# Performance work log

Hardware: AMD Instinct MI355X
Metric: run time of the kernel (lower is better)

Reference implementation:

```python
import jax, jax.numpy as jnp
import numpy as np

N, M, NTYPES, C, AXIS = 4096, 128, 2, 64, 16
TYPE_IDX = (0, 2048, 4096)        # atom-type partition along center axis
NTYPE_IDX = (0, 64, 128)          # neighbor-type partition along neighbor axis
RCUT = 6.0
BOX = 20.0
SR_MEAN = (0.1, 0.1)              # precomputed stats (get_stats)
SR_STD = (0.05, 0.05)
NORM = 20.0                       # avg neighbor count + 1


def setup_inputs() -> dict:
    key = jax.random.key(0)
    ks = jax.random.split(key, 16)
    coord_3N = jax.random.uniform(ks[0], (3, N), dtype=jnp.float32) * BOX
    box = jnp.full((3,), BOX, dtype=jnp.float32)
    # neighbors sorted by type: first 64 of type 0, last 64 of type 1
    nbr0 = jax.random.randint(ks[1], (N, M // 2), 0, TYPE_IDX[1])
    nbr1 = jax.random.randint(ks[2], (N, M // 2), TYPE_IDX[1], TYPE_IDX[2])
    nbrs_idx = jnp.concatenate([nbr0, nbr1], axis=1).astype(jnp.int32)
    # 4 per-(center,neighbor)-type embedding nets, widths 1->16->32->64, stacked
    eW0 = jax.random.normal(ks[3], (4, 1, 16), dtype=jnp.float32)
    eb0 = jax.random.normal(ks[4], (4, 16), dtype=jnp.float32) * 0.1
    eW1 = jax.random.normal(ks[5], (4, 16, 32), dtype=jnp.float32) / 4.0
    eb1 = jax.random.normal(ks[6], (4, 32), dtype=jnp.float32) * 0.1
    eW2 = jax.random.normal(ks[7], (4, 32, 64), dtype=jnp.float32) / (32.0 ** 0.5)
    eb2 = jax.random.normal(ks[8], (4, 64), dtype=jnp.float32) * 0.1
    Tbias = jnp.zeros((1, C), dtype=jnp.float32)
    # 2 per-type fitting nets, widths 1024->128->128->1, stacked
    fW0 = jax.random.normal(ks[9], (2, AXIS * C, 128), dtype=jnp.float32) / (AXIS * C) ** 0.5
    fb0 = jnp.zeros((2, 128), dtype=jnp.float32)
    fW1 = jax.random.normal(ks[10], (2, 128, 128), dtype=jnp.float32) / (128.0 ** 0.5)
    fb1 = jnp.zeros((2, 128), dtype=jnp.float32)
    fW2 = jax.random.normal(ks[11], (2, 128, 1), dtype=jnp.float32) / (128.0 ** 0.5)
    fb2 = jnp.zeros((2, 1), dtype=jnp.float32)
    Ebias = jnp.zeros((2,), dtype=jnp.float32)
    return {"coord_3N": coord_3N, "box": box, "nbrs_idx": nbrs_idx,
            "eW0": eW0, "eb0": eb0, "eW1": eW1, "eb1": eb1, "eW2": eW2, "eb2": eb2,
            "Tbias": Tbias, "fW0": fW0, "fb0": fb0, "fW1": fW1, "fb1": fb1,
            "fW2": fW2, "fb2": fb2, "Ebias": Ebias}


def reference(coord_3N, box, nbrs_idx, eW0, eb0, eW1, eb1, eW2, eb2,
              Tbias, fW0, fb0, fW1, fb1, fW2, fb2, Ebias):
    # --- neighbor gather + minimal-image relative coords (get_relative_coord) ---
    x_3NM = coord_3N[:, nbrs_idx] - coord_3N[:, :, None]            # [3,N,M]
    x_3NM = x_3NM - box[:, None, None] * jnp.round(x_3NM / box[:, None, None])
    r2 = (x_3NM ** 2).sum(0)
    mask = r2 > 1e-12
    rsafe = jnp.sqrt(jnp.where(mask, r2, 1.0))                      # safe for grads
    r_NM = jnp.where(mask, rsafe, 0.0)                              # [N,M]
    # --- smooth radial feature sr(r) = switch(r)/r ---
    sw = 0.5 * jnp.cos(jnp.pi * jnp.minimum(r_NM, RCUT) / RCUT) + 0.5
    sr_NM = jnp.where(mask & (r_NM < RCUT), sw / rsafe, 0.0)
    # --- per-center-type normalization (slice_t / concat_t over type_idx) ---
    srn_rows, srcn = [], []
    for i in range(NTYPES):
        blk = sr_NM[TYPE_IDX[i]:TYPE_IDX[i + 1]]
        srn_rows.append(blk / SR_STD[i])
        srcn.append((blk - SR_MEAN[i]) / SR_STD[i])
    sr_norm_NM = jnp.concatenate(srn_rows, 0)
    x_norm_3NM = x_3NM / jnp.where(mask, rsafe, 1.0)[None]
    R_3NM = 3 ** 0.5 * sr_norm_NM * x_norm_3NM
    R2diag_3NM = 9 ** 0.5 * sr_norm_NM * (x_norm_3NM ** 2 - 1.0 / 3.0)
    R2offd_3NM = 18 ** 0.5 * sr_norm_NM * (x_norm_3NM * jnp.stack([x_norm_3NM[1], x_norm_3NM[2], x_norm_3NM[0]]))
    R_XNM = jnp.concatenate([sr_norm_NM[None], R_3NM, R2diag_3NM, R2offd_3NM])  # [10,N,M]

    # --- per-(center,neighbor)-type embedding MLPs on scalar sr feature ---
    def embed(x, k):  # x: [n, m] -> [n, m, C]
        h = jnp.tanh(x[:, :, None] @ eW0[k] + eb0[k])
        h = jnp.tanh(h @ eW1[k] + eb1[k])
        return jnp.tanh(h @ eW2[k] + eb2[k])

    rows = []
    for i in range(NTYPES):
        cols = [embed(srcn[i][:, NTYPE_IDX[j]:NTYPE_IDX[j + 1]], i * NTYPES + j)
                for j in range(NTYPES)]
        rows.append(jnp.concatenate(cols, 1))
    embed_NMC = jnp.concatenate(rows, 0)                            # [N,M,C]

    # --- descriptor contraction ---
    T_NXC = jnp.einsum('xnm,nmc->nxc', R_XNM, embed_NMC) / NORM     # [N,10,C]
    T_NC = T_NXC[:, 0] + Tbias
    T_N3C = T_NXC[:, 1:4]
    T_N6C = T_NXC[:, 4:]
    G_NAC = T_NC[:, None] * T_NC[:, :AXIS, None] \
        + (T_N3C[:, :, None] * T_N3C[:, :, :AXIS, None]).sum(1)     # [N,AXIS,C]
    # use_2nd branch
    G1 = T_N3C[:, :, AXIS:2 * AXIS]                                 # [N,3,AXIS]
    G11 = jnp.concatenate([G1 ** 2,
                           2 ** 0.5 * G1 * jnp.stack([G1[:, 1], G1[:, 2], G1[:, 0]], axis=1)], axis=1)
    G2 = G11 + T_N6C[:, :, AXIS:2 * AXIS]                           # [N,6,AXIS]
    G_NAC = G_NAC + jnp.einsum('nxa,nxc->nac', G2, T_N6C)

    # --- per-type fitting nets ---
    Gflat = G_NAC.reshape(N, AXIS * C)
    energy = jnp.zeros((), dtype=Gflat.dtype)
    for t in range(NTYPES):
        g = Gflat[TYPE_IDX[t]:TYPE_IDX[t + 1]]
        h = jnp.tanh(g @ fW0[t] + fb0[t])
        h = jnp.tanh(h @ fW1[t] + fb1[t])
        f = h @ fW2[t] + fb2[t]
        energy = energy + (f + Ebias[t]).sum()
    return energy
```

## Files before the change

kernel.cpp:

```cpp
#include <hip/hip_runtime.h>
#include <hip/hip_fp16.h>

typedef _Float16 h16;
typedef h16 v2h __attribute__((ext_vector_type(2)));
typedef h16 v8h __attribute__((ext_vector_type(8)));
typedef float f4 __attribute__((ext_vector_type(4)));

#define NATOM 4096
#define HALF_N 2048
#define K2 2.885390081777927f
#define GSCL 0.015625f
#define W0SCL (64.0f * K2)

#define TBL_N 2048
#define W0MIN_ (-0.201f)
#define DW_ (1.2005f / 2047.0f)
#define RSCALE_ (2047.0f / 1.2005f)

__device__ __forceinline__ float rcp_fast(float x) {
#if __has_builtin(__builtin_amdgcn_rcpf)
  return __builtin_amdgcn_rcpf(x);
#else
  return 1.0f / x;
#endif
}

__device__ __forceinline__ float exp2_fast(float x) {
#if __has_builtin(__builtin_amdgcn_exp2f)
  return __builtin_amdgcn_exp2f(x);
#else
  return exp2f(x);
#endif
}

__device__ __forceinline__ float tanh_e2(float d) {
  float r = rcp_fast(1.0f + exp2_fast(d));
  return fmaf(-2.0f, r, 1.0f);
}

__device__ __forceinline__ v8h lds_v8h(const h16* base, int byte) {
  return *(const v8h*)((const char*)base + byte);
}

__global__ __launch_bounds__(256) void k_setup(
    const float* __restrict__ eW0, const float* __restrict__ eb0,
    const float* __restrict__ eW1, const float* __restrict__ eb1,
    const float* __restrict__ eW2, const float* __restrict__ eb2,
    const float* __restrict__ fW0, const float* __restrict__ fW1,
    const float* __restrict__ coord,
    h16* __restrict__ tbl, h16* __restrict__ W0t, h16* __restrict__ W1t,
    f4* __restrict__ coordP)
{
  const int bid = blockIdx.x, tid = threadIdx.x;
  if (bid < 512) {
    __shared__ float sW1[512];
    __shared__ float sW2[2048];
    __shared__ float sW0s[16], sb0s[16], sb1s[32], sb2s[64];
    const int net = bid >> 7;
    for (int i = tid; i < 512; i += 256) sW1[i] = eW1[net * 512 + i];
    for (int i = tid; i < 2048; i += 256) sW2[i] = eW2[net * 2048 + i];
    if (tid < 16) { sW0s[tid] = eW0[net * 16 + tid]; sb0s[tid] = eb0[net * 16 + tid]; }
    else if (tid >= 32 && tid < 64) sb1s[tid - 32] = eb1[net * 32 + tid - 32];
    else if (tid >= 64 && tid < 128) sb2s[tid - 64] = eb2[net * 64 + tid - 64];
    __syncthreads();

    const int u = (bid & 127) * 256 + tid;
    const int e = u >> 4, cq = u & 15;
    const float w = W0MIN_ + (float)e * DW_;
    const float s = 8.0f * w * rcp_fast(1.0f - fabsf(w));
    float h0[16];
#pragma unroll
    for (int i = 0; i < 16; ++i)
      h0[i] = tanh_e2(K2 * fmaf(s, sW0s[i], sb0s[i]));
    float h1[32];
#pragma unroll
    for (int j = 0; j < 32; ++j) {
      float a = sb1s[j];
#pragma unroll
      for (int i = 0; i < 16; ++i) a = fmaf(h0[i], sW1[i * 32 + j], a);
      h1[j] = tanh_e2(K2 * a);
    }
    f4 a4 = *(const f4*)&sb2s[cq * 4];
    for (int j = 0; j < 32; ++j) {
      f4 wv4 = *(const f4*)&sW2[j * 64 + cq * 4];
      a4 += h1[j] * wv4;
    }
    union { h16 e4[4]; unsigned long long q; } o;
#pragma unroll
    for (int q = 0; q < 4; ++q) o.e4[q] = (h16)tanh_e2(K2 * a4[q]);
    *(unsigned long long*)&tbl[((size_t)(net * TBL_N + e)) * 64 + cq * 4] = o.q;
  } else if (bid < 640) {
    int idx = (bid - 512) * 256 + tid;
    int t = idx >> 14, n = idx & 127, k8 = (idx >> 7) & 127;
    union { v8h v; h16 e[8]; } o;
#pragma unroll
    for (int i = 0; i < 8; ++i)
      o.e[i] = (h16)(W0SCL * fW0[(size_t)t * 131072 + (size_t)(k8 * 8 + i) * 128 + n]);
    *(v8h*)&W0t[((size_t)t * 128 + n) * 1024 + k8 * 8] = o.v;
  } else if (bid < 656) {
    int idx = (bid - 640) * 256 + tid;
    f4 c;
    c.x = coord[idx]; c.y = coord[NATOM + idx]; c.z = coord[2 * NATOM + idx];
    c.w = 0.0f;
    coordP[idx] = c;
  } else {
    int idx = (bid - 656) * 256 + tid;
    int t = idx >> 11, rem = idx & 2047;
    int n = rem >> 4, k8 = rem & 15;
    union { v8h v; h16 e[8]; } o;
#pragma unroll
    for (int i = 0; i < 8; ++i)
      o.e[i] = (h16)(K2 * fW1[(size_t)t * 16384 + (size_t)(k8 * 8 + i) * 128 + n]);
    *(v8h*)&W1t[((size_t)t * 128 + n) * 128 + k8 * 8] = o.v;
  }
}

__global__ __launch_bounds__(256, 2) void k_embed(
    const f4* __restrict__ coordP, const float* __restrict__ box,
    const int* __restrict__ nbrs, const float* __restrict__ Tbias,
    const h16* __restrict__ tbl, h16* __restrict__ Gout)
{
  __shared__ h16   E32t[4][64][40] __attribute__((aligned(16)));
  __shared__ h16   Rls[4][10][136] __attribute__((aligned(16)));
  __shared__ float Tls[4][10][64];

  const int tid = threadIdx.x;
  const int wv = tid >> 6;
  const int lane = tid & 63;
  const int n = blockIdx.x * 4 + wv;
  const int ti = (n >= HALF_N) ? 1 : 0;
  const int c15 = lane & 15, g4 = lane >> 4;
  const int mloc = lane >> 1, hh = lane & 1;

  const int jnb0 = nbrs[(size_t)n * 128 + lane];
  const int jnb1 = nbrs[(size_t)n * 128 + 64 + lane];

  int uf0 = 0, uf1 = 0;
  {
    const float bx = box[0], by = box[1], bz = box[2];
    const float rbx = rcp_fast(bx), rby = rcp_fast(by), rbz = rcp_fast(bz);
    const f4 cme = coordP[n];
#pragma unroll
    for (int nb = 0; nb < 2; ++nb) {
      const int m = nb * 64 + lane;
      const f4 cj = coordP[nb ? jnb1 : jnb0];
      float dx = cj.x - cme.x;
      float dy = cj.y - cme.y;
      float dz = cj.z - cme.z;
      dx -= bx * rintf(dx * rbx);
      dy -= by * rintf(dy * rby);
      dz -= bz * rintf(dz * rbz);
      float r2 = dx * dx + dy * dy + dz * dz;
      bool mk = r2 > 1e-12f;
      float rs = sqrtf(mk ? r2 : 1.0f);
      float r  = mk ? rs : 0.0f;
      float sw = 0.5f * __cosf(0.52359878f * fminf(r, 6.0f)) + 0.5f;
      float invr = mk ? rcp_fast(rs) : 1.0f;
      float sr = (mk && r < 6.0f) ? sw * invr : 0.0f;
      float x0 = dx * invr, x1 = dy * invr, x2 = dz * invr;
      float srn = sr * 20.0f;
      float s   = (sr - 0.1f) * 20.0f;
      Rls[wv][0][m] = (h16)srn;
      Rls[wv][1][m] = (h16)(1.7320508f * srn * x0);
      Rls[wv][2][m] = (h16)(1.7320508f * srn * x1);
      Rls[wv][3][m] = (h16)(1.7320508f * srn * x2);
      Rls[wv][4][m] = (h16)(3.0f * srn * (x0 * x0 - 0.33333334f));
      Rls[wv][5][m] = (h16)(3.0f * srn * (x1 * x1 - 0.33333334f));
      Rls[wv][6][m] = (h16)(3.0f * srn * (x2 * x2 - 0.33333334f));
      Rls[wv][7][m] = (h16)(4.2426407f * srn * (x0 * x1));
      Rls[wv][8][m] = (h16)(4.2426407f * srn * (x1 * x2));
      Rls[wv][9][m] = (h16)(4.2426407f * srn * (x2 * x0));
      float wr = s * rcp_fast(8.0f + fabsf(s));
      float fidx = (wr - W0MIN_) * RSCALE_;
      fidx = fminf(fmaxf(fidx, 0.0f), 2045.99f);
      float i0f = floorf(fidx);
      h16 frh = (h16)(fidx - i0f);
      int uf = ((int)i0f << 16) |
               (int)__builtin_bit_cast(unsigned short, frh);
      if (nb == 0) uf0 = uf; else uf1 = uf;
    }
  }

  union U8 { v8h v; v2h p[4]; h16 e[8]; };
  const int rrow = (c15 < 10) ? c15 : 9;
  const v8h vzero = {};
  f4 tac[4];
#pragma unroll
  for (int nt = 0; nt < 4; ++nt) tac[nt] = (f4){0.f, 0.f, 0.f, 0.f};

  auto issue = [&](int ks, U8* buf) -> float {
    unsigned uu = (unsigned)__builtin_amdgcn_ds_bpermute(
        (((ks & 1) * 32) + mloc) * 4, (ks < 2) ? uf0 : uf1);
    int i0 = (int)(uu >> 16);
    float fr = (float)__builtin_bit_cast(h16, (unsigned short)(uu & 0xffffu));
    const int net = ti * 2 + (ks >> 1);
    const h16* rp = tbl + ((size_t)net * TBL_N + i0) * 64 + hh * 8;
#pragma unroll
    for (int q = 0; q < 4; ++q) {
      buf[q].v     = *(const v8h*)(rp + q * 16);
      buf[4 + q].v = *(const v8h*)(rp + 64 + q * 16);
    }
    return fr;
  };

  auto proc = [&](int ks, U8* buf, float fr) {
    v2h fr2; fr2.x = (h16)fr; fr2.y = (h16)fr;
#pragma unroll
    for (int q = 0; q < 4; ++q) {
#pragma unroll
      for (int p = 0; p < 4; ++p) {
        v2h d = buf[4 + q].p[p] - buf[q].p[p];
        v2h e2 = buf[q].p[p] + fr2 * d;
        const int ch = q * 16 + hh * 8 + p * 2;
        E32t[wv][ch][mloc]     = e2.x;
        E32t[wv][ch + 1][mloc] = e2.y;
      }
    }
    v8h ra = *(const v8h*)&Rls[wv][rrow][ks * 32 + g4 * 8];
    if (c15 >= 10) ra = vzero;
#pragma unroll
    for (int nt = 0; nt < 4; ++nt) {
      v8h bf = *(const v8h*)&E32t[wv][nt * 16 + c15][g4 * 8];
      tac[nt] = __builtin_amdgcn_mfma_f32_16x16x32_f16(ra, bf, tac[nt], 0, 0, 0);
    }
  };

  U8 bA[8], bB[8];
  float frA = issue(0, bA);
  float frB = issue(1, bB);
  proc(0, bA, frA);
  frA = issue(2, bA);
  proc(1, bB, frB);
  frB = issue(3, bB);
  proc(2, bA, frA);
  proc(3, bB, frB);

#pragma unroll
  for (int nt = 0; nt < 4; ++nt)
#pragma unroll
    for (int r = 0; r < 4; ++r) {
      int x = g4 * 4 + r;
      if (x < 10) Tls[wv][x][nt * 16 + c15] = tac[nt][r] * 0.05f;
    }

  {
    const int c = lane;
    const float tnc  = Tls[wv][0][c] + Tbias[c];
    const float t3c0 = Tls[wv][1][c], t3c1 = Tls[wv][2][c], t3c2 = Tls[wv][3][c];
    const float t6c0 = Tls[wv][4][c], t6c1 = Tls[wv][5][c], t6c2 = Tls[wv][6][c];
    const float t6c3 = Tls[wv][7][c], t6c4 = Tls[wv][8][c], t6c5 = Tls[wv][9][c];
    h16* gp = Gout + (size_t)n * 1024;
#pragma unroll
    for (int a = 0; a < 16; ++a) {
      float g = tnc * (Tls[wv][0][a] + Tbias[a]);
      g += t3c0 * Tls[wv][1][a] + t3c1 * Tls[wv][2][a] + t3c2 * Tls[wv][3][a];
      const float g1x = Tls[wv][1][16 + a], g1y = Tls[wv][2][16 + a], g1z = Tls[wv][3][16 + a];
      g += (g1x * g1x + Tls[wv][4][16 + a]) * t6c0;
      g += (g1y * g1y + Tls[wv][5][16 + a]) * t6c1;
      g += (g1z * g1z + Tls[wv][6][16 + a]) * t6c2;
      g += (1.4142135f * g1x * g1y + Tls[wv][7][16 + a]) * t6c3;
      g += (1.4142135f * g1y * g1z + Tls[wv][8][16 + a]) * t6c4;
      g += (1.4142135f * g1z * g1x + Tls[wv][9][16 + a]) * t6c5;
      gp[a * 64 + c] = (h16)(g * GSCL);
    }
  }
}

__global__ __launch_bounds__(256) void k_fit(
    const h16* __restrict__ G16, const h16* __restrict__ W0t,
    const h16* __restrict__ W1t,
    const float* __restrict__ fb0, const float* __restrict__ fb1,
    const float* __restrict__ fW2, const float* __restrict__ fb2,
    const float* __restrict__ Ebias, float* __restrict__ BP)
{
  __shared__ h16 As[2][32][64]  __attribute__((aligned(16)));
  __shared__ h16 Bs[2][128][64] __attribute__((aligned(16)));
  __shared__ h16 ht[32][128]    __attribute__((aligned(16)));
  __shared__ h16 W1s[128][128]  __attribute__((aligned(16)));
  __shared__ float red[32][33];

  const int tid = threadIdx.x;
  const int abase = blockIdx.x * 32;
  const int t = (abase >= HALF_N) ? 1 : 0;
  const int lane = tid & 63, w = tid >> 6;
  const int c15 = lane & 15, g4 = lane >> 4;
  const int rt = w & 1, ng = w >> 1;

  float fb0v[4], b1v[4], w2v[4];
#pragma unroll
  for (int nt = 0; nt < 4; ++nt) {
    const int nn = ng * 64 + nt * 16 + c15;
    fb0v[nt] = K2 * fb0[t * 128 + nn];
    b1v[nt]  = K2 * fb1[t * 128 + nn];
    w2v[nt]  = fW2[t * 128 + nn];
  }

#pragma unroll
  for (int u = 0; u < 8; ++u) {
    int idx = u * 256 + tid;
    int nrow = idx >> 4, c8 = idx & 15;
    v8h v = *(const v8h*)&W1t[((size_t)t * 128 + nrow) * 128 + c8 * 8];
    int byte = nrow * 256 + ((c8 * 16) ^ ((nrow & 7) << 4));
    *(v8h*)((char*)&W1s[0][0] + byte) = v;
  }

  f4 acc[4];
#pragma unroll
  for (int nt = 0; nt < 4; ++nt) acc[nt] = (f4){0.f, 0.f, 0.f, 0.f};

  auto stageK = [&](int kc, int p) {
    {
      int r = tid >> 3, c8 = tid & 7;
      v8h v = *(const v8h*)&G16[(size_t)(abase + r) * 1024 + kc * 64 + c8 * 8];
      int byte = r * 128 + ((c8 * 16) ^ ((r & 7) << 4));
      *(v8h*)((char*)&As[p][0][0] + byte) = v;
    }
#pragma unroll
    for (int u = 0; u < 4; ++u) {
      int idx = u * 256 + tid;
      int nrow = idx >> 3, c8 = idx & 7;
      v8h v = *(const v8h*)&W0t[((size_t)t * 128 + nrow) * 1024 + kc * 64 + c8 * 8];
      int byte = nrow * 128 + ((c8 * 16) ^ ((nrow & 7) << 4));
      *(v8h*)((char*)&Bs[p][0][0] + byte) = v;
    }
  };

  stageK(0, 0);
  __syncthreads();
  for (int kc = 0; kc < 16; ++kc) {
    const int p = kc & 1;
    if (kc < 15) stageK(kc + 1, p ^ 1);
#pragma unroll
    for (int ksub = 0; ksub < 2; ++ksub) {
      const int ar = rt * 16 + c15;
      const int koff = (ksub * 32 + g4 * 8) * 2;
      v8h a = lds_v8h(&As[p][0][0], ar * 128 + (koff ^ ((ar & 7) << 4)));
#pragma unroll
      for (int nt = 0; nt < 4; ++nt) {
        const int br = ng * 64 + nt * 16 + c15;
        v8h b = lds_v8h(&Bs[p][0][0], br * 128 + (koff ^ ((br & 7) << 4)));
        acc[nt] = __builtin_amdgcn_mfma_f32_16x16x32_f16(a, b, acc[nt], 0, 0, 0);
      }
    }
    __syncthreads();
  }

#pragma unroll
  for (int nt = 0; nt < 4; ++nt)
#pragma unroll
    for (int r = 0; r < 4; ++r) {
      int a = rt * 16 + g4 * 4 + r;
      int k = ng * 64 + nt * 16 + c15;
      h16 hv = (h16)tanh_e2(acc[nt][r] + fb0v[nt]);
      int byte = a * 256 + ((k * 2) ^ ((a & 7) << 4));
      *((h16*)((char*)&ht[0][0] + byte)) = hv;
    }
  __syncthreads();

  f4 acc2[4];
#pragma unroll
  for (int nt = 0; nt < 4; ++nt) acc2[nt] = (f4){0.f, 0.f, 0.f, 0.f};
#pragma unroll
  for (int ks2 = 0; ks2 < 4; ++ks2) {
    const int ar = rt * 16 + c15;
    const int koff = (ks2 * 32 + g4 * 8) * 2;
    v8h a = lds_v8h(&ht[0][0], ar * 256 + (koff ^ ((ar & 7) << 4)));
#pragma unroll
    for (int nt = 0; nt < 4; ++nt) {
      const int br = ng * 64 + nt * 16 + c15;
      v8h b = lds_v8h(&W1s[0][0], br * 256 + (koff ^ ((br & 7) << 4)));
      acc2[nt] = __builtin_amdgcn_mfma_f32_16x16x32_f16(a, b, acc2[nt], 0, 0, 0);
    }
  }

#pragma unroll
  for (int r = 0; r < 4; ++r) {
    float v = 0.0f;
#pragma unroll
    for (int nt = 0; nt < 4; ++nt)
      v += tanh_e2(acc2[nt][r] + b1v[nt]) * w2v[nt];
    red[rt * 16 + g4 * 4 + r][ng * 16 + c15] = v;
  }
  __syncthreads();
  if (tid < 64) {
    const int a = tid & 31, half = tid >> 5;
    float s = 0.0f;
#pragma unroll
    for (int c = 0; c < 16; ++c) s += red[a][half * 16 + c];
    s += __shfl_xor(s, 32);
    s += __shfl_xor(s, 16);
    s += __shfl_xor(s, 8);
    s += __shfl_xor(s, 4);
    s += __shfl_xor(s, 2);
    s += __shfl_xor(s, 1);
    if (tid == 0) BP[blockIdx.x] = s + 32.0f * (fb2[t] + Ebias[t]);
  }
}

__global__ __launch_bounds__(64) void k_reduce(const float* __restrict__ BP,
                                               float* __restrict__ out)
{
  int tid = threadIdx.x;
  float s = BP[tid] + BP[tid + 64];
  s += __shfl_xor(s, 32);
  s += __shfl_xor(s, 16);
  s += __shfl_xor(s, 8);
  s += __shfl_xor(s, 4);
  s += __shfl_xor(s, 2);
  s += __shfl_xor(s, 1);
  if (tid == 0) out[0] = s;
}

extern "C" void kernel_launch(void* const* d_in, const int* in_sizes, int n_in,
                              void* d_out, int out_size, void* d_ws, size_t ws_size,
                              hipStream_t stream) {
  const float* coord = (const float*)d_in[0];
  const float* box   = (const float*)d_in[1];
  const int*   nbrs  = (const int*)d_in[2];
  const float* eW0   = (const float*)d_in[3];
  const float* eb0   = (const float*)d_in[4];
  const float* eW1   = (const float*)d_in[5];
  const float* eb1   = (const float*)d_in[6];
  const float* eW2   = (const float*)d_in[7];
  const float* eb2   = (const float*)d_in[8];
  const float* Tbias = (const float*)d_in[9];
  const float* fW0   = (const float*)d_in[10];
  const float* fb0   = (const float*)d_in[11];
  const float* fW1   = (const float*)d_in[12];
  const float* fb1   = (const float*)d_in[13];
  const float* fW2   = (const float*)d_in[14];
  const float* fb2   = (const float*)d_in[15];
  const float* Ebias = (const float*)d_in[16];

  char* ws = (char*)d_ws;
  h16*   G16 = (h16*)ws;
  h16*   W0t = (h16*)(ws + (size_t)8  * 1024 * 1024);
  h16*   W1t = (h16*)(ws + (size_t)9  * 1024 * 1024);
  h16*   tbl = (h16*)(ws + (size_t)10 * 1024 * 1024);
  f4*    cP  = (f4*)(ws + (size_t)11 * 1024 * 1024);
  float* BP  = (float*)(ws + (size_t)12 * 1024 * 1024);

  k_setup<<<672, 256, 0, stream>>>(eW0, eb0, eW1, eb1, eW2, eb2, fW0, fW1,
                                   coord, tbl, W0t, W1t, cP);
  k_embed<<<1024, 256, 0, stream>>>(cP, box, nbrs, Tbias, tbl, G16);
  k_fit<<<128, 256, 0, stream>>>(G16, W0t, W1t, fb0, fb1, fW2, fb2, Ebias, BP);
  k_reduce<<<1, 64, 0, stream>>>(BP, (float*)d_out);
}
```

Before: 44.84 us.

## Compute G descriptor contraction with MFMA and shrink embed kernel LDS footprint

The per-atom G = T^T·U contraction (16x64 from 10 inner terms) moves from a scalar FP32 loop over LDS into a single-wave fp16 MFMA. T and a scaled U matrix are packed into reused LDS pools. LDS is consolidated into two per-wave pools, occupancy is raised to 4 blocks per CU, and the table interpolation is remapped so each lane handles two neighbors and 16 channels, allowing paired v2h stores. The tradeoff is extra fp16 rounding of T and U, which needs the USCL scaling to stay in range.

```diff
diff --git a/kernel.cpp b/kernel.cpp
--- a/kernel.cpp
+++ b/kernel.cpp
@@ -3,6 +3,7 @@
 
 typedef _Float16 h16;
 typedef h16 v2h __attribute__((ext_vector_type(2)));
+typedef h16 v4h __attribute__((ext_vector_type(4)));
 typedef h16 v8h __attribute__((ext_vector_type(8)));
 typedef float f4 __attribute__((ext_vector_type(4)));
 
@@ -11,6 +12,8 @@
 #define K2 2.885390081777927f
 #define GSCL 0.015625f
 #define W0SCL (64.0f * K2)
+#define USCL 0.0625f
+#define GOUTS (GSCL / USCL)
 
 #define TBL_N 2048
 #define W0MIN_ (-0.201f)
@@ -115,14 +118,13 @@
   }
 }
 
-__global__ __launch_bounds__(256, 2) void k_embed(
+__global__ __launch_bounds__(256, 4) void k_embed(
     const f4* __restrict__ coordP, const float* __restrict__ box,
     const int* __restrict__ nbrs, const float* __restrict__ Tbias,
     const h16* __restrict__ tbl, h16* __restrict__ Gout)
 {
-  __shared__ h16   E32t[4][64][40] __attribute__((aligned(16)));
-  __shared__ h16   Rls[4][10][136] __attribute__((aligned(16)));
-  __shared__ float Tls[4][10][64];
+  __shared__ h16 pool1[4][2560] __attribute__((aligned(16)));
+  __shared__ h16 pool2[4][1360] __attribute__((aligned(16)));
 
   const int tid = threadIdx.x;
   const int wv = tid >> 6;
@@ -130,7 +132,10 @@
   const int n = blockIdx.x * 4 + wv;
   const int ti = (n >= HALF_N) ? 1 : 0;
   const int c15 = lane & 15, g4 = lane >> 4;
-  const int mloc = lane >> 1, hh = lane & 1;
+  const int mp = lane >> 2, cg = lane & 3;
+
+  h16* E32 = &pool1[wv][0];
+  h16* Rl  = &pool2[wv][0];
 
   const int jnb0 = nbrs[(size_t)n * 128 + lane];
   const int jnb1 = nbrs[(size_t)n * 128 + 64 + lane];
@@ -160,16 +165,16 @@
       float x0 = dx * invr, x1 = dy * invr, x2 = dz * invr;
       float srn = sr * 20.0f;
       float s   = (sr - 0.1f) * 20.0f;
-      Rls[wv][0][m] = (h16)srn;
-      Rls[wv][1][m] = (h16)(1.7320508f * srn * x0);
-      Rls[wv][2][m] = (h16)(1.7320508f * srn * x1);
-      Rls[wv][3][m] = (h16)(1.7320508f * srn * x2);
-      Rls[wv][4][m] = (h16)(3.0f * srn * (x0 * x0 - 0.33333334f));
-      Rls[wv][5][m] = (h16)(3.0f * srn * (x1 * x1 - 0.33333334f));
-      Rls[wv][6][m] = (h16)(3.0f * srn * (x2 * x2 - 0.33333334f));
-      Rls[wv][7][m] = (h16)(4.2426407f * srn * (x0 * x1));
-      Rls[wv][8][m] = (h16)(4.2426407f * srn * (x1 * x2));
-      Rls[wv][9][m] = (h16)(4.2426407f * srn * (x2 * x0));
+      Rl[0 * 136 + m] = (h16)srn;
+      Rl[1 * 136 + m] = (h16)(1.7320508f * srn * x0);
+      Rl[2 * 136 + m] = (h16)(1.7320508f * srn * x1);
+      Rl[3 * 136 + m] = (h16)(1.7320508f * srn * x2);
+      Rl[4 * 136 + m] = (h16)(3.0f * srn * (x0 * x0 - 0.33333334f));
+      Rl[5 * 136 + m] = (h16)(3.0f * srn * (x1 * x1 - 0.33333334f));
+      Rl[6 * 136 + m] = (h16)(3.0f * srn * (x2 * x2 - 0.33333334f));
+      Rl[7 * 136 + m] = (h16)(4.2426407f * srn * (x0 * x1));
+      Rl[8 * 136 + m] = (h16)(4.2426407f * srn * (x1 * x2));
+      Rl[9 * 136 + m] = (h16)(4.2426407f * srn * (x2 * x0));
       float wr = s * rcp_fast(8.0f + fabsf(s));
       float fidx = (wr - W0MIN_) * RSCALE_;
       fidx = fminf(fmaxf(fidx, 0.0f), 2045.99f);
@@ -188,80 +193,117 @@
 #pragma unroll
   for (int nt = 0; nt < 4; ++nt) tac[nt] = (f4){0.f, 0.f, 0.f, 0.f};
 
-  auto issue = [&](int ks, U8* buf) -> float {
-    unsigned uu = (unsigned)__builtin_amdgcn_ds_bpermute(
-        (((ks & 1) * 32) + mloc) * 4, (ks < 2) ? uf0 : uf1);
-    int i0 = (int)(uu >> 16);
-    float fr = (float)__builtin_bit_cast(h16, (unsigned short)(uu & 0xffffu));
-    const int net = ti * 2 + (ks >> 1);
-    const h16* rp = tbl + ((size_t)net * TBL_N + i0) * 64 + hh * 8;
-#pragma unroll
-    for (int q = 0; q < 4; ++q) {
-      buf[q].v     = *(const v8h*)(rp + q * 16);
-      buf[4 + q].v = *(const v8h*)(rp + 64 + q * 16);
-    }
-    return fr;
+  auto issue = [&](int ks, U8* buf, float* fr) {
+#pragma unroll
+    for (int e = 0; e < 2; ++e) {
+      int src = ((ks & 1) * 32 + mp * 2 + e) * 4;
+      unsigned uu = (unsigned)__builtin_amdgcn_ds_bpermute(src, (ks < 2) ? uf0 : uf1);
+      int i0 = (int)(uu >> 16);
+      fr[e] = (float)__builtin_bit_cast(h16, (unsigned short)(uu & 0xffffu));
+      const int net = ti * 2 + (ks >> 1);
+      const h16* rp = tbl + ((size_t)net * TBL_N + i0) * 64 + cg * 16;
+      buf[e * 4 + 0].v = *(const v8h*)(rp);
+      buf[e * 4 + 1].v = *(const v8h*)(rp + 8);
+      buf[e * 4 + 2].v = *(const v8h*)(rp + 64);
+      buf[e * 4 + 3].v = *(const v8h*)(rp + 72);
+    }
   };
 
-  auto proc = [&](int ks, U8* buf, float fr) {
-    v2h fr2; fr2.x = (h16)fr; fr2.y = (h16)fr;
-#pragma unroll
-    for (int q = 0; q < 4; ++q) {
+  auto proc = [&](int ks, U8* buf, const float* fr) {
+    v2h f0; f0.x = (h16)fr[0]; f0.y = (h16)fr[0];
+    v2h f1; f1.x = (h16)fr[1]; f1.y = (h16)fr[1];
+    const int m0 = mp * 2;
+#pragma unroll
+    for (int ch8 = 0; ch8 < 2; ++ch8) {
 #pragma unroll
       for (int p = 0; p < 4; ++p) {
-        v2h d = buf[4 + q].p[p] - buf[q].p[p];
-        v2h e2 = buf[q].p[p] + fr2 * d;
-        const int ch = q * 16 + hh * 8 + p * 2;
-        E32t[wv][ch][mloc]     = e2.x;
-        E32t[wv][ch + 1][mloc] = e2.y;
+        v2h e0 = buf[ch8].p[p]     + f0 * (buf[2 + ch8].p[p] - buf[ch8].p[p]);
+        v2h e1 = buf[4 + ch8].p[p] + f1 * (buf[6 + ch8].p[p] - buf[4 + ch8].p[p]);
+        const int c = cg * 16 + ch8 * 8 + p * 2;
+        v2h w0; w0.x = e0.x; w0.y = e1.x;
+        v2h w1; w1.x = e0.y; w1.y = e1.y;
+        *(v2h*)&E32[c * 40 + m0]       = w0;
+        *(v2h*)&E32[(c + 1) * 40 + m0] = w1;
       }
     }
-    v8h ra = *(const v8h*)&Rls[wv][rrow][ks * 32 + g4 * 8];
+    v8h ra = *(const v8h*)&Rl[rrow * 136 + ks * 32 + g4 * 8];
     if (c15 >= 10) ra = vzero;
 #pragma unroll
     for (int nt = 0; nt < 4; ++nt) {
-      v8h bf = *(const v8h*)&E32t[wv][nt * 16 + c15][g4 * 8];
+      v8h bf = *(const v8h*)&E32[(nt * 16 + c15) * 40 + g4 * 8];
       tac[nt] = __builtin_amdgcn_mfma_f32_16x16x32_f16(ra, bf, tac[nt], 0, 0, 0);
     }
   };
 
   U8 bA[8], bB[8];
-  float frA = issue(0, bA);
-  float frB = issue(1, bB);
+  float frA[2], frB[2];
+  issue(0, bA, frA);
+  issue(1, bB, frB);
   proc(0, bA, frA);
-  frA = issue(2, bA);
+  issue(2, bA, frA);
   proc(1, bB, frB);
-  frB = issue(3, bB);
+  issue(3, bB, frB);
   proc(2, bA, frA);
   proc(3, bB, frB);
 
-#pragma unroll
-  for (int nt = 0; nt < 4; ++nt)
-#pragma unroll
-    for (int r = 0; r < 4; ++r) {
-      int x = g4 * 4 + r;
-      if (x < 10) Tls[wv][x][nt * 16 + c15] = tac[nt][r] * 0.05f;
-    }
+  h16* Vt = E32;
+  h16* Ul = Rl;
+#pragma unroll
+  for (int nt = 0; nt < 4; ++nt) {
+    const int col = nt * 16 + c15;
+    float tb = (g4 == 0) ? Tbias[col] : 0.0f;
+    v4h pk;
+    pk[0] = (h16)(tac[nt][0] * 0.05f + tb);
+    pk[1] = (h16)(tac[nt][1] * 0.05f);
+    pk[2] = (h16)(tac[nt][2] * 0.05f);
+    pk[3] = (h16)(tac[nt][3] * 0.05f);
+    *(v4h*)&Vt[col * 40 + g4 * 4] = pk;
+  }
+  *(v8h*)&Vt[lane * 40 + 16] = vzero;
+  *(v8h*)&Vt[lane * 40 + 24] = vzero;
+
+  if (lane < 16) {
+    const h16* va = &Vt[lane * 40];
+    const h16* vb = &Vt[(16 + lane) * 40];
+    v8h Ta = *(const v8h*)va;
+    v8h Tb = *(const v8h*)vb;
+    v2h Tb8 = *(const v2h*)(vb + 8);
+    float g1x = (float)Tb[1], g1y = (float)Tb[2], g1z = (float)Tb[3];
+    v8h up;
+    up[0] = (h16)((float)Ta[0] * USCL);
+    up[1] = (h16)((float)Ta[1] * USCL);
+    up[2] = (h16)((float)Ta[2] * USCL);
+    up[3] = (h16)((float)Ta[3] * USCL);
+    up[4] = (h16)((g1x * g1x + (float)Tb[4]) * USCL);
+    up[5] = (h16)((g1y * g1y + (float)Tb[5]) * USCL);
+    up[6] = (h16)((g1z * g1z + (float)Tb[6]) * USCL);
+    up[7] = (h16)((1.4142135f * g1x * g1y + (float)Tb[7]) * USCL);
+    *(v8h*)&Ul[lane * 40] = up;
+    v2h u89;
+    u89.x = (h16)((1.4142135f * g1y * g1z + (float)Tb8[0]) * USCL);
+    u89.y = (h16)((1.4142135f * g1z * g1x + (float)Tb8[1]) * USCL);
+    *(v2h*)&Ul[lane * 40 + 8] = u89;
+    v2h z2 = {};
+    v4h z4 = {};
+    *(v2h*)&Ul[lane * 40 + 10] = z2;
+    *(v4h*)&Ul[lane * 40 + 12] = z4;
+    *(v8h*)&Ul[lane * 40 + 16] = vzero;
+    *(v8h*)&Ul[lane * 40 + 24] = vzero;
+  }
 
   {
-    const int c = lane;
-    const float tnc  = Tls[wv][0][c] + Tbias[c];
-    const float t3c0 = Tls[wv][1][c], t3c1 = Tls[wv][2][c], t3c2 = Tls[wv][3][c];
-    const float t6c0 = Tls[wv][4][c], t6c1 = Tls[wv][5][c], t6c2 = Tls[wv][6][c];
-    const float t6c3 = Tls[wv][7][c], t6c4 = Tls[wv][8][c], t6c5 = Tls[wv][9][c];
+    v8h ua = *(const v8h*)&Ul[c15 * 40 + g4 * 8];
     h16* gp = Gout + (size_t)n * 1024;
 #pragma unroll
-    for (int a = 0; a < 16; ++a) {
-      float g = tnc * (Tls[wv][0][a] + Tbias[a]);
-      g += t3c0 * Tls[wv][1][a] + t3c1 * Tls[wv][2][a] + t3c2 * Tls[wv][3][a];
-      const float g1x = Tls[wv][1][16 + a], g1y = Tls[wv][2][16 + a], g1z = Tls[wv][3][16 + a];
-      g += (g1x * g1x + Tls[wv][4][16 + a]) * t6c0;
-      g += (g1y * g1y + Tls[wv][5][16 + a]) * t6c1;
-      g += (g1z * g1z + Tls[wv][6][16 + a]) * t6c2;
-      g += (1.4142135f * g1x * g1y + Tls[wv][7][16 + a]) * t6c3;
-      g += (1.4142135f * g1y * g1z + Tls[wv][8][16 + a]) * t6c4;
-      g += (1.4142135f * g1z * g1x + Tls[wv][9][16 + a]) * t6c5;
-      gp[a * 64 + c] = (h16)(g * GSCL);
+    for (int nt = 0; nt < 4; ++nt) {
+      v8h vb = *(const v8h*)&Vt[(nt * 16 + c15) * 40 + g4 * 8];
+      f4 z = (f4){0.f, 0.f, 0.f, 0.f};
+      f4 g = __builtin_amdgcn_mfma_f32_16x16x32_f16(ua, vb, z, 0, 0, 0);
+#pragma unroll
+      for (int r = 0; r < 4; ++r) {
+        const int a = g4 * 4 + r;
+        gp[a * 64 + nt * 16 + c15] = (h16)(g[r] * GOUTS);
+      }
     }
   }
 }
```

Result: faster. 42.70 us (-4.8%).
